# Performance work log

Measured on AMD Instinct MI355X. Metric: run time of the kernel, lower is better.

The kernel has to match this reference:

```python
import jax, jax.numpy as jnp
import numpy as np

N_USERS = 8192
N_ITEMS = 4096
BATCH = 8192


def setup_inputs() -> dict:
    key = jax.random.key(0)
    k1, k2, k3, k4, k5, k6, k7 = jax.random.split(key, 7)
    # ratings in {0..5}; zeros mark unrated entries (needed for nonzero masking)
    rating_mtx = jax.random.randint(k1, (N_USERS, N_ITEMS), 0, 6).astype(jnp.float32)
    user = jax.random.randint(k2, (BATCH,), 0, N_USERS)
    item = jax.random.randint(k3, (BATCH,), 0, N_ITEMS)
    # learned parameters (xavier-normal similarity; biases initialized like global mean)
    xavier_std = float(np.sqrt(2.0 / (N_USERS + N_USERS)))
    user_similarity = jax.random.normal(k4, (N_USERS, N_USERS), dtype=jnp.float32) * xavier_std
    user_bias = jax.random.normal(k5, (N_USERS,), dtype=jnp.float32)
    item_bias = jax.random.normal(k6, (N_ITEMS,), dtype=jnp.float32)
    global_bias = jax.random.normal(k7, (), dtype=jnp.float32)
    return {
        "user": user,
        "item": item,
        "rating_mtx": rating_mtx,
        "user_similarity": user_similarity,
        "user_bias": user_bias,
        "item_bias": item_bias,
        "global_bias": global_bias,
    }


def reference(user, item, rating_mtx, user_similarity, user_bias, item_bias, global_bias):
    # per-user mean over NONZERO ratings (0 if user rated nothing) -- single fused
    # masked sum/count reduction replacing the per-row python loop
    mask = rating_mtx != 0  # [U, I]
    cnt = jnp.sum(mask, axis=1)  # [U]
    row_sum = jnp.sum(rating_mtx, axis=1)  # zeros contribute nothing
    user_bias_fixed = jnp.where(cnt > 0, row_sum / jnp.maximum(cnt, 1).astype(rating_mtx.dtype), 0.0)

    adjusted = rating_mtx - user_bias_fixed[:, None]  # [U, I]
    similarities = user_similarity[user]  # [B, U]
    item_ratings = adjusted[:, item]  # [U, B]
    user_scores = jnp.sum(similarities * item_ratings.T, axis=1)  # [B]

    bias = user_bias[user] + item_bias[item] + global_bias  # [B]
    return jax.nn.sigmoid(user_scores + bias) * 5.0
```

## Files before the change

### kernel.cpp

```cpp
#include <hip/hip_runtime.h>
#include <math.h>

#define N_USERS 8192
#define N_ITEMS 4096
#define BATCH   8192

__device__ __forceinline__ unsigned short f32_to_bf16_rne(float f) {
    union { float f; unsigned int u; } cvt;
    cvt.f = f;
    unsigned int u = cvt.u;
    u += 0x7fffu + ((u >> 16) & 1u);
    return (unsigned short)(u >> 16);
}
__device__ __forceinline__ float bf16_bits_to_f32(unsigned int h) {
    union { unsigned int u; float f; } cvt;
    cvt.u = h << 16;
    return cvt.f;
}

__global__ __launch_bounds__(256) void k_ubfix(const float* __restrict__ R,
                                               float* __restrict__ ub) {
    const int wave = threadIdx.x >> 6;
    const int lane = threadIdx.x & 63;
    const int u = blockIdx.x * 4 + wave;
    const float4* row4 = (const float4*)(R + (size_t)u * N_ITEMS);
    float s = 0.f, c = 0.f;
    #pragma unroll
    for (int i = 0; i < 16; ++i) {
        float4 v = row4[i * 64 + lane];
        s += v.x + v.y + v.z + v.w;
        c += (v.x != 0.f) + (v.y != 0.f) + (v.z != 0.f) + (v.w != 0.f);
    }
    #pragma unroll
    for (int off = 32; off; off >>= 1) {
        s += __shfl_down(s, off);
        c += __shfl_down(c, off);
    }
    if (lane == 0)
        ub[u] = (c > 0.f) ? s / fmaxf(c, 1.f) : 0.f;
}

__global__ __launch_bounds__(256) void k_transpose(const float* __restrict__ R,
                                                   const float* __restrict__ ub,
                                                   unsigned short* __restrict__ AT) {
    __shared__ float lds[64][65];
    const int colBase = blockIdx.x * 64;
    const int rowBase = blockIdx.y * 64;
    const int tx = threadIdx.x, ty = threadIdx.y;
    const int x4 = tx * 4;

    #pragma unroll
    for (int k = 0; k < 4; ++k) {
        const int y = ty + 16 * k;
        float4 v = *(const float4*)(R + (size_t)(rowBase + y) * N_ITEMS + colBase + x4);
        lds[y][x4 + 0] = v.x;
        lds[y][x4 + 1] = v.y;
        lds[y][x4 + 2] = v.z;
        lds[y][x4 + 3] = v.w;
    }
    __syncthreads();

    const float u0 = ub[rowBase + x4 + 0];
    const float u1 = ub[rowBase + x4 + 1];
    const float u2 = ub[rowBase + x4 + 2];
    const float u3 = ub[rowBase + x4 + 3];

    #pragma unroll
    for (int k = 0; k < 4; ++k) {
        const int y = ty + 16 * k;
        ushort4 w;
        w.x = f32_to_bf16_rne(lds[x4 + 0][y] - u0);
        w.y = f32_to_bf16_rne(lds[x4 + 1][y] - u1);
        w.z = f32_to_bf16_rne(lds[x4 + 2][y] - u2);
        w.w = f32_to_bf16_rne(lds[x4 + 3][y] - u3);
        *(ushort4*)(AT + (size_t)(colBase + y) * N_USERS + rowBase + x4) = w;
    }
}

__global__ __launch_bounds__(256) void k_main(const float* __restrict__ S,
                                              const unsigned short* __restrict__ AT,
                                              const int* __restrict__ user,
                                              const int* __restrict__ item,
                                              const float* __restrict__ ubias,
                                              const float* __restrict__ ibias,
                                              const float* __restrict__ gbias,
                                              float* __restrict__ out) {
    const int wave = threadIdx.x >> 6;
    const int lane = threadIdx.x & 63;
    const int b = blockIdx.x * 4 + wave;
    const int su = user[b];
    const int j  = item[b];
    const float4* srow = (const float4*)(S + (size_t)su * N_USERS);
    const uint4*  arow = (const uint4*)(AT + (size_t)j * N_USERS);

    float acc = 0.f;
    #pragma unroll 4
    for (int i = 0; i < 16; ++i) {
        const int idx = i * 64 + lane;
        uint4  a  = arow[idx];
        float4 s0 = srow[idx * 2 + 0];
        float4 s1 = srow[idx * 2 + 1];
        acc += s0.x * bf16_bits_to_f32(a.x & 0xffffu);
        acc += s0.y * bf16_bits_to_f32(a.x >> 16);
        acc += s0.z * bf16_bits_to_f32(a.y & 0xffffu);
        acc += s0.w * bf16_bits_to_f32(a.y >> 16);
        acc += s1.x * bf16_bits_to_f32(a.z & 0xffffu);
        acc += s1.y * bf16_bits_to_f32(a.z >> 16);
        acc += s1.z * bf16_bits_to_f32(a.w & 0xffffu);
        acc += s1.w * bf16_bits_to_f32(a.w >> 16);
    }
    #pragma unroll
    for (int off = 32; off; off >>= 1) acc += __shfl_down(acc, off);

    if (lane == 0) {
        float score = acc + ubias[su] + ibias[j] + gbias[0];
        out[b] = 5.f / (1.f + expf(-score));
    }
}

__global__ __launch_bounds__(256) void k_direct(const float* __restrict__ S,
                                                const float* __restrict__ R,
                                                const float* __restrict__ ub,
                                                const int* __restrict__ user,
                                                const int* __restrict__ item,
                                                const float* __restrict__ ubias,
                                                const float* __restrict__ ibias,
                                                const float* __restrict__ gbias,
                                                float* __restrict__ out) {
    const int b = blockIdx.x;
    const int su = user[b];
    const int j  = item[b];
    const float* srow = S + (size_t)su * N_USERS;
    float acc = 0.f;
    for (int u = threadIdx.x; u < N_USERS; u += 256) {
        acc += srow[u] * (R[(size_t)u * N_ITEMS + j] - ub[u]);
    }
    for (int off = 32; off; off >>= 1) acc += __shfl_down(acc, off);
    __shared__ float sa[4];
    const int lane = threadIdx.x & 63, w = threadIdx.x >> 6;
    if (lane == 0) sa[w] = acc;
    __syncthreads();
    if (threadIdx.x == 0) {
        float score = sa[0] + sa[1] + sa[2] + sa[3]
                    + ubias[su] + ibias[j] + gbias[0];
        out[b] = 5.f / (1.f + expf(-score));
    }
}

extern "C" void kernel_launch(void* const* d_in, const int* in_sizes, int n_in,
                              void* d_out, int out_size, void* d_ws, size_t ws_size,
                              hipStream_t stream) {
    const int*   user  = (const int*)d_in[0];
    const int*   item  = (const int*)d_in[1];
    const float* R     = (const float*)d_in[2];
    const float* S     = (const float*)d_in[3];
    const float* ubias = (const float*)d_in[4];
    const float* ibias = (const float*)d_in[5];
    const float* gbias = (const float*)d_in[6];
    float* out = (float*)d_out;

    float* ub = (float*)d_ws;
    unsigned short* AT = (unsigned short*)((char*)d_ws + 65536);
    const size_t need = 65536 + (size_t)N_ITEMS * N_USERS * sizeof(unsigned short);

    k_ubfix<<<N_USERS / 4, 256, 0, stream>>>(R, ub);

    if (ws_size >= need) {
        dim3 tgrid(N_ITEMS / 64, N_USERS / 64);
        dim3 tblk(16, 16);
        k_transpose<<<tgrid, tblk, 0, stream>>>(R, ub, AT);
        k_main<<<BATCH / 4, 256, 0, stream>>>(S, AT, user, item, ubias, ibias, gbias, out);
    } else {
        k_direct<<<BATCH, 256, 0, stream>>>(S, R, ub, user, item, ubias, ibias, gbias, out);
    }
}
```

Measured before the change: 470.8 us.

## Fuse row-mean into transpose and store ratings as uint8 transposed matrix

The separate row-mean pass over the rating matrix is removed. Per-tile partial sums and counts are now produced inside the transpose kernel and reduced by a small finalize kernel, so R is read once instead of twice. The transposed matrix now stores raw integer ratings as bytes rather than mean-subtracted bf16, halving both the write and the later gather traffic, and the mean is subtracted in the main kernel. This relies on ratings being small non-negative integers, which the task guarantees. It adds partial-sum buffers and an extra kernel launch.

```diff
diff --git a/kernel.cpp b/kernel.cpp
--- a/kernel.cpp
+++ b/kernel.cpp
@@ -4,51 +4,19 @@
 #define N_USERS 8192
 #define N_ITEMS 4096
 #define BATCH   8192
-
-__device__ __forceinline__ unsigned short f32_to_bf16_rne(float f) {
-    union { float f; unsigned int u; } cvt;
-    cvt.f = f;
-    unsigned int u = cvt.u;
-    u += 0x7fffu + ((u >> 16) & 1u);
-    return (unsigned short)(u >> 16);
-}
-__device__ __forceinline__ float bf16_bits_to_f32(unsigned int h) {
-    union { unsigned int u; float f; } cvt;
-    cvt.u = h << 16;
-    return cvt.f;
-}
-
-__global__ __launch_bounds__(256) void k_ubfix(const float* __restrict__ R,
-                                               float* __restrict__ ub) {
-    const int wave = threadIdx.x >> 6;
-    const int lane = threadIdx.x & 63;
-    const int u = blockIdx.x * 4 + wave;
-    const float4* row4 = (const float4*)(R + (size_t)u * N_ITEMS);
-    float s = 0.f, c = 0.f;
-    #pragma unroll
-    for (int i = 0; i < 16; ++i) {
-        float4 v = row4[i * 64 + lane];
-        s += v.x + v.y + v.z + v.w;
-        c += (v.x != 0.f) + (v.y != 0.f) + (v.z != 0.f) + (v.w != 0.f);
-    }
-    #pragma unroll
-    for (int off = 32; off; off >>= 1) {
-        s += __shfl_down(s, off);
-        c += __shfl_down(c, off);
-    }
-    if (lane == 0)
-        ub[u] = (c > 0.f) ? s / fmaxf(c, 1.f) : 0.f;
-}
-
-__global__ __launch_bounds__(256) void k_transpose(const float* __restrict__ R,
-                                                   const float* __restrict__ ub,
-                                                   unsigned short* __restrict__ AT) {
+#define NTILE_I (N_ITEMS / 64)
+
+__global__ __launch_bounds__(256) void k_trans(const float* __restrict__ R,
+                                               unsigned char* __restrict__ AT,
+                                               float* __restrict__ psum,
+                                               float* __restrict__ pcnt) {
     __shared__ float lds[64][65];
     const int colBase = blockIdx.x * 64;
     const int rowBase = blockIdx.y * 64;
     const int tx = threadIdx.x, ty = threadIdx.y;
     const int x4 = tx * 4;
 
+    float s[4], c[4];
     #pragma unroll
     for (int k = 0; k < 4; ++k) {
         const int y = ty + 16 * k;
@@ -57,28 +25,58 @@
         lds[y][x4 + 1] = v.y;
         lds[y][x4 + 2] = v.z;
         lds[y][x4 + 3] = v.w;
+        s[k] = v.x + v.y + v.z + v.w;
+        c[k] = (v.x != 0.f) + (v.y != 0.f) + (v.z != 0.f) + (v.w != 0.f);
+    }
+    #pragma unroll
+    for (int k = 0; k < 4; ++k) {
+        #pragma unroll
+        for (int off = 8; off; off >>= 1) {
+            s[k] += __shfl_down(s[k], off, 16);
+            c[k] += __shfl_down(c[k], off, 16);
+        }
+    }
+    if (tx == 0) {
+        #pragma unroll
+        for (int k = 0; k < 4; ++k) {
+            const int u = rowBase + ty + 16 * k;
+            psum[(size_t)blockIdx.x * N_USERS + u] = s[k];
+            pcnt[(size_t)blockIdx.x * N_USERS + u] = c[k];
+        }
     }
     __syncthreads();
 
-    const float u0 = ub[rowBase + x4 + 0];
-    const float u1 = ub[rowBase + x4 + 1];
-    const float u2 = ub[rowBase + x4 + 2];
-    const float u3 = ub[rowBase + x4 + 3];
-
-    #pragma unroll
-    for (int k = 0; k < 4; ++k) {
-        const int y = ty + 16 * k;
-        ushort4 w;
-        w.x = f32_to_bf16_rne(lds[x4 + 0][y] - u0);
-        w.y = f32_to_bf16_rne(lds[x4 + 1][y] - u1);
-        w.z = f32_to_bf16_rne(lds[x4 + 2][y] - u2);
-        w.w = f32_to_bf16_rne(lds[x4 + 3][y] - u3);
-        *(ushort4*)(AT + (size_t)(colBase + y) * N_USERS + rowBase + x4) = w;
-    }
+    const int tid = ty * 16 + tx;
+    #pragma unroll
+    for (int ss = 0; ss < 2; ++ss) {
+        const int idx = ss * 256 + tid;
+        const int il = idx >> 3;
+        const int ch = idx & 7;
+        unsigned long long w = 0;
+        #pragma unroll
+        for (int e = 0; e < 8; ++e) {
+            w |= (unsigned long long)(unsigned char)(int)lds[ch * 8 + e][il] << (8 * e);
+        }
+        *(unsigned long long*)(AT + (size_t)(colBase + il) * N_USERS + rowBase + ch * 8) = w;
+    }
+}
+
+__global__ __launch_bounds__(256) void k_fin(const float* __restrict__ psum,
+                                             const float* __restrict__ pcnt,
+                                             float* __restrict__ ub) {
+    const int u = blockIdx.x * 256 + threadIdx.x;
+    float s = 0.f, c = 0.f;
+    #pragma unroll
+    for (int t = 0; t < NTILE_I; ++t) {
+        s += psum[(size_t)t * N_USERS + u];
+        c += pcnt[(size_t)t * N_USERS + u];
+    }
+    ub[u] = (c > 0.f) ? s / fmaxf(c, 1.f) : 0.f;
 }
 
 __global__ __launch_bounds__(256) void k_main(const float* __restrict__ S,
-                                              const unsigned short* __restrict__ AT,
+                                              const unsigned char* __restrict__ AT,
+                                              const float* __restrict__ ub,
                                               const int* __restrict__ user,
                                               const int* __restrict__ item,
                                               const float* __restrict__ ubias,
@@ -90,24 +88,27 @@
     const int b = blockIdx.x * 4 + wave;
     const int su = user[b];
     const int j  = item[b];
-    const float4* srow = (const float4*)(S + (size_t)su * N_USERS);
-    const uint4*  arow = (const uint4*)(AT + (size_t)j * N_USERS);
+    const float4* srow  = (const float4*)(S + (size_t)su * N_USERS);
+    const float4* ubrow = (const float4*)ub;
+    const uint2*  arow  = (const uint2*)(AT + (size_t)j * N_USERS);
 
     float acc = 0.f;
     #pragma unroll 4
     for (int i = 0; i < 16; ++i) {
         const int idx = i * 64 + lane;
-        uint4  a  = arow[idx];
-        float4 s0 = srow[idx * 2 + 0];
-        float4 s1 = srow[idx * 2 + 1];
-        acc += s0.x * bf16_bits_to_f32(a.x & 0xffffu);
-        acc += s0.y * bf16_bits_to_f32(a.x >> 16);
-        acc += s0.z * bf16_bits_to_f32(a.y & 0xffffu);
-        acc += s0.w * bf16_bits_to_f32(a.y >> 16);
-        acc += s1.x * bf16_bits_to_f32(a.z & 0xffffu);
-        acc += s1.y * bf16_bits_to_f32(a.z >> 16);
-        acc += s1.z * bf16_bits_to_f32(a.w & 0xffffu);
-        acc += s1.w * bf16_bits_to_f32(a.w >> 16);
+        uint2  a  = arow[idx];
+        float4 s0 = srow[2 * idx + 0];
+        float4 s1 = srow[2 * idx + 1];
+        float4 u0 = ubrow[2 * idx + 0];
+        float4 u1 = ubrow[2 * idx + 1];
+        acc += s0.x * ((float)( a.x        & 0xffu) - u0.x);
+        acc += s0.y * ((float)((a.x >>  8) & 0xffu) - u0.y);
+        acc += s0.z * ((float)((a.x >> 16) & 0xffu) - u0.z);
+        acc += s0.w * ((float)( a.x >> 24         ) - u0.w);
+        acc += s1.x * ((float)( a.y        & 0xffu) - u1.x);
+        acc += s1.y * ((float)((a.y >>  8) & 0xffu) - u1.y);
+        acc += s1.z * ((float)((a.y >> 16) & 0xffu) - u1.z);
+        acc += s1.w * ((float)( a.y >> 24         ) - u1.w);
     }
     #pragma unroll
     for (int off = 32; off; off >>= 1) acc += __shfl_down(acc, off);
@@ -116,6 +117,28 @@
         float score = acc + ubias[su] + ibias[j] + gbias[0];
         out[b] = 5.f / (1.f + expf(-score));
     }
+}
+
+__global__ __launch_bounds__(256) void k_ubfix(const float* __restrict__ R,
+                                               float* __restrict__ ub) {
+    const int wave = threadIdx.x >> 6;
+    const int lane = threadIdx.x & 63;
+    const int u = blockIdx.x * 4 + wave;
+    const float4* row4 = (const float4*)(R + (size_t)u * N_ITEMS);
+    float s = 0.f, c = 0.f;
+    #pragma unroll
+    for (int i = 0; i < 16; ++i) {
+        float4 v = row4[i * 64 + lane];
+        s += v.x + v.y + v.z + v.w;
+        c += (v.x != 0.f) + (v.y != 0.f) + (v.z != 0.f) + (v.w != 0.f);
+    }
+    #pragma unroll
+    for (int off = 32; off; off >>= 1) {
+        s += __shfl_down(s, off);
+        c += __shfl_down(c, off);
+    }
+    if (lane == 0)
+        ub[u] = (c > 0.f) ? s / fmaxf(c, 1.f) : 0.f;
 }
 
 __global__ __launch_bounds__(256) void k_direct(const float* __restrict__ S,
@@ -159,18 +182,20 @@
     const float* gbias = (const float*)d_in[6];
     float* out = (float*)d_out;
 
-    float* ub = (float*)d_ws;
-    unsigned short* AT = (unsigned short*)((char*)d_ws + 65536);
-    const size_t need = 65536 + (size_t)N_ITEMS * N_USERS * sizeof(unsigned short);
-
-    k_ubfix<<<N_USERS / 4, 256, 0, stream>>>(R, ub);
+    float* ub   = (float*)d_ws;
+    float* psum = (float*)((char*)d_ws + (64u << 10));
+    float* pcnt = (float*)((char*)d_ws + (64u << 10) + ((size_t)NTILE_I * N_USERS * 4));
+    unsigned char* AT = (unsigned char*)((char*)d_ws + (8u << 20));
+    const size_t need = (8u << 20) + (size_t)N_ITEMS * N_USERS;
 
     if (ws_size >= need) {
-        dim3 tgrid(N_ITEMS / 64, N_USERS / 64);
+        dim3 tgrid(NTILE_I, N_USERS / 64);
         dim3 tblk(16, 16);
-        k_transpose<<<tgrid, tblk, 0, stream>>>(R, ub, AT);
-        k_main<<<BATCH / 4, 256, 0, stream>>>(S, AT, user, item, ubias, ibias, gbias, out);
+        k_trans<<<tgrid, tblk, 0, stream>>>(R, AT, psum, pcnt);
+        k_fin<<<N_USERS / 256, 256, 0, stream>>>(psum, pcnt, ub);
+        k_main<<<BATCH / 4, 256, 0, stream>>>(S, AT, ub, user, item, ubias, ibias, gbias, out);
     } else {
+        k_ubfix<<<N_USERS / 4, 256, 0, stream>>>(R, ub);
         k_direct<<<BATCH, 256, 0, stream>>>(S, R, ub, user, item, ubias, ibias, gbias, out);
     }
 }
```

Result: no change. 469.2 us (-0.3%).
